# Optimization experiments

Hardware: AMD Instinct MI355X
Metric: run time of the kernel (lower is better)

The kernel has to match this reference:

```python
import jax, jax.numpy as jnp
import numpy as np
from jax.scipy.special import digamma, gammaln

B, NQ, NK, DM = 8, 2048, 2048, 64
NEG = -1e9


def setup_inputs() -> dict:
    key = jax.random.key(0)
    ks = jax.random.split(key, 9)
    y = jax.random.normal(ks[0], (B, NQ, DM), dtype=jnp.float32)
    x = jax.random.normal(ks[1], (B, NK, DM), dtype=jnp.float32)
    mask = jnp.ones((B, NQ, NK), dtype=jnp.float32)
    eps = jax.random.normal(ks[2], (B, NQ, NK), dtype=jnp.float32)
    # stacked 3-layer MLP params (all layers are DM x DM since d_q=d_k=d_v=d_m)
    Wq = jax.random.normal(ks[3], (3, DM, DM), dtype=jnp.float32) * 0.1
    bq = jnp.zeros((3, DM), dtype=jnp.float32)
    Wk = jax.random.normal(ks[4], (3, DM, DM), dtype=jnp.float32) * 0.1
    bk = jnp.zeros((3, DM), dtype=jnp.float32)
    Wv = jax.random.normal(ks[5], (3, DM, DM), dtype=jnp.float32) * 0.1
    bv = jnp.zeros((3, DM), dtype=jnp.float32)
    return {"y": y, "x": x, "mask": mask, "eps": eps,
            "Wq": Wq, "bq": bq, "Wk": Wk, "bk": bk, "Wv": Wv, "bv": bv}


def _mlp(h, W, b, last_softplus):
    # 3-layer MLP; softplus after first two layers, optionally after last
    for i in range(3):
        h = h @ W[i] + b[i]
        if i < 2 or last_softplus:
            h = jax.nn.softplus(h)
    return h


def _dirichlet_kld(alpha, mask):
    a0 = (alpha * mask).sum(-1, keepdims=True)
    dg_a = digamma(alpha)
    dg_a0 = digamma(a0)
    kl = (gammaln(a0)
          - (gammaln(alpha) * mask).sum(-1, keepdims=True)
          + (alpha * dg_a * mask).sum(-1, keepdims=True)
          - (alpha * dg_a0 * mask).sum(-1, keepdims=True)
          - ((dg_a - dg_a0) * mask).mean(-1, keepdims=True))
    return jnp.abs(kl)


def reference(y, x, mask, eps, Wq, bq, Wk, bk, Wv, bv):
    q = _mlp(y, Wq, bq, True)          # [B,NQ,DM]
    k = _mlp(x, Wk, bk, True)          # [B,NK,DM]
    va = _mlp(x, Wv, bv, False)        # [B,NK,DM]
    qk = jnp.einsum('bqd,bkd->bqk', q, k)
    alpha = qk + 1.0                   # > 1, safe for log/digamma
    log_alpha = jnp.log(alpha)
    mu = (log_alpha - (log_alpha * mask).mean(-1, keepdims=True)) * mask
    latent = mask.sum(-1, keepdims=True)
    inv_a = 1.0 / alpha
    sigma = ((1.0 - 2.0 / latent) * inv_a
             + (1.0 / latent ** 2) * (inv_a * mask).sum(-1, keepdims=True)) * mask
    kld = _dirichlet_kld(alpha, mask).mean()
    neg = (1.0 - mask) * NEG
    attn = jax.nn.softmax(mu + sigma * eps + neg, axis=-1)
    out = attn @ va                    # [B,NQ,DM]
    return out, attn, va, kld
```

## Files before the change

### kernel.cpp

```cpp
#include <hip/hip_runtime.h>
#include <cstdint>
#include <cstddef>

#define BB 8
#define NQ 2048
#define NK 2048
#define DM 64
#define QT 16
#define TPB 512
#define PST 2056

typedef float    f4    __attribute__((ext_vector_type(4)));
typedef short    s16x8 __attribute__((ext_vector_type(8)));
typedef unsigned u32x2 __attribute__((ext_vector_type(2)));
typedef unsigned u32x4 __attribute__((ext_vector_type(4)));

__device__ __forceinline__ float frcp(float x){
  float r = __builtin_amdgcn_rcpf(x);
  return r * (2.0f - x*r);
}
__device__ __forceinline__ float softplus(float v){
  return fmaxf(v, 0.0f) + log1pf(__expf(-fabsf(v)));
}
__device__ __forceinline__ float bflo(unsigned u){ return __uint_as_float(u << 16); }
__device__ __forceinline__ float bfhi(unsigned u){ return __uint_as_float(u & 0xffff0000u); }
__device__ __forceinline__ unsigned short f2bf(float f){
  unsigned u = __float_as_uint(f);
  return (unsigned short)((u + 0x7fffu + ((u >> 16) & 1u)) >> 16);
}
__device__ __forceinline__ unsigned pack_rne(float lo, float hi){
  return (unsigned)f2bf(lo) | ((unsigned)f2bf(hi) << 16);
}
__device__ __forceinline__ float red32(float v){
  #pragma unroll
  for (int s = 1; s < 32; s <<= 1) v += __shfl_xor(v, s);
  return v;
}

__global__ __launch_bounds__(256) void mlp3_kernel(
    const float* __restrict__ y, const float* __restrict__ x,
    const float* __restrict__ Wq, const float* __restrict__ bq,
    const float* __restrict__ Wk, const float* __restrict__ bk,
    const float* __restrict__ Wv, const float* __restrict__ bv,
    unsigned short* __restrict__ qo, unsigned short* __restrict__ ko,
    float* __restrict__ vo, unsigned short* __restrict__ vaT){
  const int which = blockIdx.y;
  const float* src = (which == 0) ? y : x;
  const float* W   = (which == 0) ? Wq : (which == 1 ? Wk : Wv);
  const float* bb  = (which == 0) ? bq : (which == 1 ? bk : bv);
  const int row0 = blockIdx.x * 64;
  const int t = threadIdx.x;
  const int lane = t & 63, w = t >> 6, lm = lane & 15, lg = lane >> 4;

  __shared__ unsigned short Xl[64][72];
  __shared__ unsigned short Wt[64][72];
  __shared__ float bl[64];

  #pragma unroll
  for (int p = 0; p < 4; ++p){
    int idx = t + p*256;
    int r = idx >> 4, c4 = idx & 15;
    f4 v = ((const f4*)(src + (size_t)row0*DM))[idx];
    u32x2 o = { pack_rne(v.x, v.y), pack_rne(v.z, v.w) };
    *(u32x2*)&Xl[r][c4*4] = o;
  }

  const int wr = w * 16;
  for (int l = 0; l < 3; ++l){
    __syncthreads();
    #pragma unroll
    for (int p = 0; p < 4; ++p){
      int idx = t + p*256;
      int k = idx >> 4, c4 = idx & 15;
      f4 v = ((const f4*)(W + l*DM*DM))[idx];
      Wt[c4*4+0][k] = f2bf(v.x);
      Wt[c4*4+1][k] = f2bf(v.y);
      Wt[c4*4+2][k] = f2bf(v.z);
      Wt[c4*4+3][k] = f2bf(v.w);
    }
    if (t < 64) bl[t] = bb[l*DM + t];
    __syncthreads();
    const bool sp = (l < 2) || (which != 2);
    s16x8 a0 = *(const s16x8*)&Xl[wr + lm][lg*8];
    s16x8 a1 = *(const s16x8*)&Xl[wr + lm][32 + lg*8];
    f4 outv[4];
    #pragma unroll
    for (int nt = 0; nt < 4; ++nt){
      s16x8 b0 = *(const s16x8*)&Wt[nt*16 + lm][lg*8];
      s16x8 b1 = *(const s16x8*)&Wt[nt*16 + lm][32 + lg*8];
      f4 acc = {0.f, 0.f, 0.f, 0.f};
      acc = __builtin_amdgcn_mfma_f32_16x16x32_bf16(a0, b0, acc, 0, 0, 0);
      acc = __builtin_amdgcn_mfma_f32_16x16x32_bf16(a1, b1, acc, 0, 0, 0);
      const float bc = bl[nt*16 + lm];
      #pragma unroll
      for (int r = 0; r < 4; ++r){
        float vv = acc[r] + bc;
        if (sp) vv = softplus(vv);
        acc[r] = vv;
      }
      outv[nt] = acc;
    }
    #pragma unroll
    for (int nt = 0; nt < 4; ++nt)
      #pragma unroll
      for (int r = 0; r < 4; ++r)
        Xl[wr + lg*4 + r][nt*16 + lm] = f2bf(outv[nt][r]);
  }
  __syncthreads();

  if (which != 2){
    unsigned short* dst = ((which == 0) ? qo : ko) + (size_t)row0*DM;
    #pragma unroll
    for (int p = 0; p < 4; ++p){
      int idx = t + p*256;
      int r = idx >> 4, c4 = idx & 15;
      u32x2 u = *(const u32x2*)&Xl[r][c4*4];
      *(u32x2*)(dst + (size_t)idx*4) = u;
    }
  } else {
    #pragma unroll
    for (int p = 0; p < 4; ++p){
      int idx = t + p*256;
      int r = idx >> 4, c4 = idx & 15;
      u32x2 u = *(const u32x2*)&Xl[r][c4*4];
      f4 v = { bflo(u[0]), bfhi(u[0]), bflo(u[1]), bfhi(u[1]) };
      ((f4*)(vo + (size_t)row0*DM))[idx] = v;
    }
    const int bidx = row0 >> 11, jb = row0 & 2047;
    const int d = t >> 2, rs = t & 3;
    u32x4 o0, o1;
    #pragma unroll
    for (int i = 0; i < 4; ++i)
      o0[i] = (unsigned)Xl[rs*16 + 2*i][d] | ((unsigned)Xl[rs*16 + 2*i + 1][d] << 16);
    #pragma unroll
    for (int i = 0; i < 4; ++i)
      o1[i] = (unsigned)Xl[rs*16 + 8 + 2*i][d] | ((unsigned)Xl[rs*16 + 9 + 2*i][d] << 16);
    unsigned short* dst = vaT + ((size_t)bidx*DM + d)*NK + jb + rs*16;
    *(u32x4*)dst       = o0;
    *(u32x4*)(dst + 8) = o1;
  }
}

__global__ __launch_bounds__(TPB, 4) void bayes_main_kernel(
    const unsigned short* __restrict__ qbf, const unsigned short* __restrict__ kbf,
    const unsigned short* __restrict__ vaT,
    const float* __restrict__ maskg, const float* __restrict__ epsg,
    float* __restrict__ outg, float* __restrict__ attng, float* __restrict__ klws){
  const int b  = blockIdx.x & 7;
  const int qt = blockIdx.x >> 3;
  const int q0 = qt * QT;
  const int t  = threadIdx.x;
  const int lane = t & 63, w = t >> 6;
  const int lm = lane & 15, lg = lane >> 4;

  __shared__ unsigned short Plds[QT][PST];
  __shared__ float pvred[4][QT][16];
  __shared__ float rowinvL[QT], klrow[QT];

  {
    const unsigned short* qrow = qbf + ((size_t)(b*NQ + q0 + lm))*DM + lg*8;
    s16x8 qa0 = *(const s16x8*)qrow;
    s16x8 qa1 = *(const s16x8*)(qrow + 32);
    #pragma unroll 2
    for (int tt = 0; tt < 16; ++tt){
      const int jt = w*16 + tt;
      const unsigned short* krow = kbf + ((size_t)(b*NK + jt*16 + lm))*DM + lg*8;
      s16x8 kb0 = *(const s16x8*)krow;
      s16x8 kb1 = *(const s16x8*)(krow + 32);
      f4 acc = {0.f, 0.f, 0.f, 0.f};
      acc = __builtin_amdgcn_mfma_f32_16x16x32_bf16(qa0, kb0, acc, 0, 0, 0);
      acc = __builtin_amdgcn_mfma_f32_16x16x32_bf16(qa1, kb1, acc, 0, 0, 0);
      #pragma unroll
      for (int r = 0; r < 4; ++r)
        Plds[lg*4 + r][jt*16 + lm] = f2bf(acc[r]);
    }
  }
  __syncthreads();

  const int row = t >> 5, c = t & 31;
  const size_t rowoff = ((size_t)(b*NQ) + q0 + row)*NK;

  float a0 = 0, Sg = 0, Sadg = 0, Sdg = 0, Sinv = 0, lat = 0;
  unsigned long long mbits = 0;
  #pragma unroll
  for (int h = 0; h < 2; ++h){
    f4 pm[8];
    #pragma unroll
    for (int k = 0; k < 8; ++k)
      pm[k] = *(const f4*)(maskg + rowoff + (h*8 + k)*128 + c*4);
    #pragma unroll
    for (int k = 0; k < 8; ++k){
      const int kk = h*8 + k;
      u32x2 sw = *(const u32x2*)&Plds[row][kk*128 + c*4];
      const float av[4] = { bflo(sw[0]) + 1.0f, bfhi(sw[0]) + 1.0f,
                            bflo(sw[1]) + 1.0f, bfhi(sw[1]) + 1.0f };
      #pragma unroll
      for (int c4 = 0; c4 < 4; ++c4){
        float a = av[c4], m = pm[k][c4];
        if (m != 0.0f) mbits |= 1ull << (kk*4 + c4);
        float inv = __builtin_amdgcn_rcpf(a);
        float la  = __logf(a);
        float xs  = a + 1.0f;
        float lxs = __logf(xs);
        float rxs = __builtin_amdgcn_rcpf(xs);
        float rx2 = rxs*rxs;
        float t1  = fmaf(-rx2, 1.0f/252.0f, 1.0f/120.0f);
        float t2  = fmaf(-rx2, t1, 1.0f/12.0f);
        float psi = fmaf(-rx2, t2, fmaf(-0.5f, rxs, lxs)) - inv;
        float u1  = fmaf(-rx2, 1.0f/1260.0f, 1.0f/360.0f);
        float u2  = fmaf(-rx2, u1, 1.0f/12.0f);
        float lg2 = fmaf(xs - 0.5f, lxs, fmaf(rxs, u2, 0.91893853320467274f))
                  - xs - la;
        a0   = fmaf(a,     m, a0);
        Sg   = fmaf(lg2,   m, Sg);
        Sadg = fmaf(a*psi, m, Sadg);
        Sdg  = fmaf(psi,   m, Sdg);
        Sinv = fmaf(inv,   m, Sinv);
        lat += m;
      }
    }
  }
  a0 = red32(a0); Sg = red32(Sg); Sadg = red32(Sadg);
  Sdg = red32(Sdg); Sinv = red32(Sinv); lat = red32(lat);

  const float invLT = frcp(lat);
  const float c1 = 1.0f - 2.0f*invLT;
  const float S2 = Sinv*invLT*invLT;
  if (c == 0){
    double A0d = (double)a0, csum = 0.0, prod = 1.0;
    #pragma unroll
    for (int s = 0; s < 7; ++s){
      if (A0d < 8.0){ csum += 1.0/A0d; prod *= A0d; A0d += 1.0; }
    }
    double lx = log(A0d), r1 = 1.0/A0d, r2 = r1*r1;
    double psiA = lx - 0.5*r1
                - r2*((1.0/12.0) - r2*((1.0/120.0) - r2*(1.0/252.0))) - csum;
    double lgA  = (A0d - 0.5)*lx - A0d + 0.918938533204672741
                + r1*((1.0/12.0) - r2*((1.0/360.0) - r2*(1.0/1260.0))) - log(prod);
    double kl = lgA - (double)Sg + (double)Sadg - psiA*(double)a0
              - ((double)Sdg - psiA*(double)lat)*(1.0/(double)NK);
    klrow[row] = (float)fabs(kl);
  }

  float esum = 0.0f;
  #pragma unroll
  for (int h = 0; h < 2; ++h){
    f4 pe[8];
    #pragma unroll
    for (int k = 0; k < 8; ++k)
      pe[k] = __builtin_nontemporal_load(
          (const f4*)(epsg + rowoff + (h*8 + k)*128 + c*4));
    #pragma unroll
    for (int k = 0; k < 8; ++k){
      const int kk = h*8 + k;
      u32x2 sw = *(const u32x2*)&Plds[row][kk*128 + c*4];
      const float av[4] = { bflo(sw[0]) + 1.0f, bfhi(sw[0]) + 1.0f,
                            bflo(sw[1]) + 1.0f, bfhi(sw[1]) + 1.0f };
      float e2v[4];
      #pragma unroll
      for (int c4 = 0; c4 < 4; ++c4){
        float e2 = 0.0f;
        if ((mbits >> (kk*4 + c4)) & 1ull){
          float a = av[c4];
          float sig = fmaf(c1, __builtin_amdgcn_rcpf(a), S2);
          e2 = a * __expf(sig * pe[k][c4]);
        }
        e2v[c4] = e2;
        esum += e2;
      }
      u32x2 ow = { pack_rne(e2v[0], e2v[1]), pack_rne(e2v[2], e2v[3]) };
      *(u32x2*)&Plds[row][kk*128 + c*4] = ow;
    }
  }
  esum = red32(esum);
  const float rinv = frcp(esum);
  if (c == 0) rowinvL[row] = rinv;

  #pragma unroll 4
  for (int k = 0; k < 16; ++k){
    u32x2 ew = *(const u32x2*)&Plds[row][k*128 + c*4];
    f4 o = { bflo(ew[0])*rinv, bfhi(ew[0])*rinv, bflo(ew[1])*rinv, bfhi(ew[1])*rinv };
    __builtin_nontemporal_store(o, (f4*)(attng + rowoff + k*128 + c*4));
  }
  __syncthreads();

  if (t == 0){
    float s = 0;
    #pragma unroll
    for (int r = 0; r < QT; ++r) s += klrow[r];
    klws[b*(NQ/QT) + qt] = s;
  }

  const int dt = w & 3, jh = w >> 2;
  f4 oacc = {0.f, 0.f, 0.f, 0.f};
  const unsigned short* vrow = vaT + ((size_t)(b*DM) + dt*16 + lm)*NK + jh*1024 + lg*8;
  const unsigned short* prow = &Plds[lm][jh*1024 + lg*8];
  #pragma unroll 4
  for (int ks = 0; ks < 32; ++ks){
    s16x8 pa = *(const s16x8*)(prow + ks*32);
    s16x8 vb = *(const s16x8*)(vrow + ks*32);
    oacc = __builtin_amdgcn_mfma_f32_16x16x32_bf16(pa, vb, oacc, 0, 0, 0);
  }
  if (w >= 4){
    #pragma unroll
    for (int r = 0; r < 4; ++r) pvred[dt][lg*4 + r][lm] = oacc[r];
  }
  __syncthreads();
  if (w < 4){
    #pragma unroll
    for (int r = 0; r < 4; ++r){
      const int q = lg*4 + r;
      float v = (oacc[r] + pvred[dt][q][lm]) * rowinvL[q];
      outg[((size_t)(b*NQ) + q0 + q)*DM + dt*16 + lm] = v;
    }
  }
}

__global__ __launch_bounds__(256) void kld_reduce_kernel(
    const float* __restrict__ klws, float* __restrict__ dst){
  float s = 0.0f;
  for (int i = threadIdx.x; i < BB*(NQ/QT); i += 256) s += klws[i];
  #pragma unroll
  for (int o = 32; o; o >>= 1) s += __shfl_down(s, o);
  __shared__ float w4[4];
  if ((threadIdx.x & 63) == 0) w4[threadIdx.x >> 6] = s;
  __syncthreads();
  if (threadIdx.x == 0)
    dst[0] = (w4[0] + w4[1] + w4[2] + w4[3]) * (1.0f/((float)BB*(float)NQ));
}

extern "C" void kernel_launch(void* const* d_in, const int* in_sizes, int n_in,
                              void* d_out, int out_size, void* d_ws, size_t ws_size,
                              hipStream_t stream){
  const float* y    = (const float*)d_in[0];
  const float* x    = (const float*)d_in[1];
  const float* mask = (const float*)d_in[2];
  const float* eps  = (const float*)d_in[3];
  const float* Wq   = (const float*)d_in[4];
  const float* bq   = (const float*)d_in[5];
  const float* Wk   = (const float*)d_in[6];
  const float* bk   = (const float*)d_in[7];
  const float* Wv   = (const float*)d_in[8];
  const float* bv   = (const float*)d_in[9];

  float* out  = (float*)d_out;
  float* attn = out  + (size_t)BB*NQ*DM;
  float* va   = attn + (size_t)BB*NQ*NK;
  float* kld  = va   + (size_t)BB*NK*DM;

  char* wsb = (char*)d_ws;
  unsigned short* qbf  = (unsigned short*)wsb;
  unsigned short* kbf  = (unsigned short*)(wsb + (size_t)BB*NQ*DM*2);
  unsigned short* vaT  = (unsigned short*)(wsb + (size_t)BB*NQ*DM*4);
  float*          klws = (float*)(wsb + (size_t)BB*NQ*DM*6);

  dim3 gA((BB*NQ)/64, 3);
  hipLaunchKernelGGL(mlp3_kernel, gA, dim3(256), 0, stream,
                     y, x, Wq, bq, Wk, bk, Wv, bv, qbf, kbf, va, vaT);
  hipLaunchKernelGGL(bayes_main_kernel, dim3(BB*(NQ/QT)), dim3(TPB), 0, stream,
                     qbf, kbf, vaT, mask, eps, out, attn, klws);
  hipLaunchKernelGGL(kld_reduce_kernel, dim3(1), dim3(256), 0, stream, klws, kld);
}
```

Measured before the change: 156.7 us.

## Replace per-element digamma/gammaln with aggregated Stirling sums and fold alpha+1 into bf16 store

```diff
diff --git a/kernel.cpp b/kernel.cpp
--- a/kernel.cpp
+++ b/kernel.cpp
@@ -10,6 +10,10 @@
 #define TPB 512
 #define PST 2056
 
+#define LN2f   0.6931471805599453f
+#define LOG2Ef 1.4426950408889634f
+#define HL2PIf 0.9189385332046727f
+
 typedef float    f4    __attribute__((ext_vector_type(4)));
 typedef short    s16x8 __attribute__((ext_vector_type(8)));
 typedef unsigned u32x2 __attribute__((ext_vector_type(2)));
@@ -30,6 +34,11 @@
 }
 __device__ __forceinline__ unsigned pack_rne(float lo, float hi){
   return (unsigned)f2bf(lo) | ((unsigned)f2bf(hi) << 16);
+}
+__device__ __forceinline__ unsigned cvtpk(float lo, float hi){
+  unsigned r;
+  asm("v_cvt_pk_bf16_f32 %0, %1, %2" : "=v"(r) : "v"(lo), "v"(hi));
+  return r;
 }
 __device__ __forceinline__ float red32(float v){
   #pragma unroll
@@ -170,9 +179,13 @@
       f4 acc = {0.f, 0.f, 0.f, 0.f};
       acc = __builtin_amdgcn_mfma_f32_16x16x32_bf16(qa0, kb0, acc, 0, 0, 0);
       acc = __builtin_amdgcn_mfma_f32_16x16x32_bf16(qa1, kb1, acc, 0, 0, 0);
-      #pragma unroll
-      for (int r = 0; r < 4; ++r)
-        Plds[lg*4 + r][jt*16 + lm] = f2bf(acc[r]);
+      unsigned p01 = cvtpk(acc[0] + 1.0f, acc[1] + 1.0f);
+      unsigned p23 = cvtpk(acc[2] + 1.0f, acc[3] + 1.0f);
+      const int col = jt*16 + lm;
+      Plds[lg*4 + 0][col] = (unsigned short)(p01 & 0xffffu);
+      Plds[lg*4 + 1][col] = (unsigned short)(p01 >> 16);
+      Plds[lg*4 + 2][col] = (unsigned short)(p23 & 0xffffu);
+      Plds[lg*4 + 3][col] = (unsigned short)(p23 >> 16);
     }
   }
   __syncthreads();
@@ -180,8 +193,7 @@
   const int row = t >> 5, c = t & 31;
   const size_t rowoff = ((size_t)(b*NQ) + q0 + row)*NK;
 
-  float a0 = 0, Sg = 0, Sadg = 0, Sdg = 0, Sinv = 0, lat = 0;
-  unsigned long long mbits = 0;
+  float a0 = 0, Sl2 = 0, Sinv = 0, Si2 = 0, lat = 0;
   #pragma unroll
   for (int h = 0; h < 2; ++h){
     f4 pm[8];
@@ -192,83 +204,71 @@
     for (int k = 0; k < 8; ++k){
       const int kk = h*8 + k;
       u32x2 sw = *(const u32x2*)&Plds[row][kk*128 + c*4];
-      const float av[4] = { bflo(sw[0]) + 1.0f, bfhi(sw[0]) + 1.0f,
-                            bflo(sw[1]) + 1.0f, bfhi(sw[1]) + 1.0f };
+      const float av[4] = { bflo(sw[0]), bfhi(sw[0]), bflo(sw[1]), bfhi(sw[1]) };
       #pragma unroll
       for (int c4 = 0; c4 < 4; ++c4){
         float a = av[c4], m = pm[k][c4];
-        if (m != 0.0f) mbits |= 1ull << (kk*4 + c4);
         float inv = __builtin_amdgcn_rcpf(a);
-        float la  = __logf(a);
-        float xs  = a + 1.0f;
-        float lxs = __logf(xs);
-        float rxs = __builtin_amdgcn_rcpf(xs);
-        float rx2 = rxs*rxs;
-        float t1  = fmaf(-rx2, 1.0f/252.0f, 1.0f/120.0f);
-        float t2  = fmaf(-rx2, t1, 1.0f/12.0f);
-        float psi = fmaf(-rx2, t2, fmaf(-0.5f, rxs, lxs)) - inv;
-        float u1  = fmaf(-rx2, 1.0f/1260.0f, 1.0f/360.0f);
-        float u2  = fmaf(-rx2, u1, 1.0f/12.0f);
-        float lg2 = fmaf(xs - 0.5f, lxs, fmaf(rxs, u2, 0.91893853320467274f))
-                  - xs - la;
-        a0   = fmaf(a,     m, a0);
-        Sg   = fmaf(lg2,   m, Sg);
-        Sadg = fmaf(a*psi, m, Sadg);
-        Sdg  = fmaf(psi,   m, Sdg);
-        Sinv = fmaf(inv,   m, Sinv);
+        float l2  = __builtin_amdgcn_logf(a);
+        a0   = fmaf(a,       m, a0);
+        Sl2  = fmaf(l2,      m, Sl2);
+        Sinv = fmaf(inv,     m, Sinv);
+        Si2  = fmaf(inv*inv, m, Si2);
         lat += m;
       }
     }
   }
-  a0 = red32(a0); Sg = red32(Sg); Sadg = red32(Sadg);
-  Sdg = red32(Sdg); Sinv = red32(Sinv); lat = red32(lat);
-
+  a0 = red32(a0); Sl2 = red32(Sl2); Sinv = red32(Sinv);
+  Si2 = red32(Si2); lat = red32(lat);
+
+  const float Sl = Sl2 * LN2f;
   const float invLT = frcp(lat);
   const float c1 = 1.0f - 2.0f*invLT;
   const float S2 = Sinv*invLT*invLT;
-  if (c == 0){
-    double A0d = (double)a0, csum = 0.0, prod = 1.0;
-    #pragma unroll
-    for (int s = 0; s < 7; ++s){
-      if (A0d < 8.0){ csum += 1.0/A0d; prod *= A0d; A0d += 1.0; }
-    }
-    double lx = log(A0d), r1 = 1.0/A0d, r2 = r1*r1;
-    double psiA = lx - 0.5*r1
-                - r2*((1.0/12.0) - r2*((1.0/120.0) - r2*(1.0/252.0))) - csum;
-    double lgA  = (A0d - 0.5)*lx - A0d + 0.918938533204672741
-                + r1*((1.0/12.0) - r2*((1.0/360.0) - r2*(1.0/1260.0))) - log(prod);
-    double kl = lgA - (double)Sg + (double)Sadg - psiA*(double)a0
-              - ((double)Sdg - psiA*(double)lat)*(1.0/(double)NK);
-    klrow[row] = (float)fabs(kl);
-  }
-
+  {
+    const float la0 = __builtin_amdgcn_logf(a0) * LN2f;
+    const float ra0 = frcp(a0);
+    const float ra2 = ra0*ra0;
+    const float psiA = la0 - 0.5f*ra0 - ra2*(1.0f/12.0f - ra2*(1.0f/120.0f));
+    const float lgA  = fmaf(a0 - 0.5f, la0, -a0) + HL2PIf
+                     + ra0*(1.0f/12.0f - ra2*(1.0f/360.0f));
+    const float gsum = fmaf(0.5f, Sl, a0) - lat*(0.5f + HL2PIf) - Sinv*(1.0f/6.0f);
+    const float Sdg  = Sl - 0.5f*Sinv - Si2*(1.0f/12.0f);
+    const float kl   = lgA - psiA*a0 + gsum
+                     - (Sdg - psiA*lat)*(1.0f/(float)NK);
+    if (c == 0) klrow[row] = fabsf(kl);
+  }
+
+  const float c1e = c1 * LOG2Ef, S2e = S2 * LOG2Ef;
   float esum = 0.0f;
-  #pragma unroll
-  for (int h = 0; h < 2; ++h){
-    f4 pe[8];
-    #pragma unroll
-    for (int k = 0; k < 8; ++k)
-      pe[k] = __builtin_nontemporal_load(
-          (const f4*)(epsg + rowoff + (h*8 + k)*128 + c*4));
-    #pragma unroll
-    for (int k = 0; k < 8; ++k){
-      const int kk = h*8 + k;
+  u32x2 e2pk[16];
+  #pragma unroll
+  for (int hb = 0; hb < 4; ++hb){
+    f4 pm[4], pe[4];
+    #pragma unroll
+    for (int j = 0; j < 4; ++j){
+      pm[j] = *(const f4*)(maskg + rowoff + (hb*4 + j)*128 + c*4);
+      pe[j] = __builtin_nontemporal_load(
+          (const f4*)(epsg + rowoff + (hb*4 + j)*128 + c*4));
+    }
+    #pragma unroll
+    for (int j = 0; j < 4; ++j){
+      const int kk = hb*4 + j;
       u32x2 sw = *(const u32x2*)&Plds[row][kk*128 + c*4];
-      const float av[4] = { bflo(sw[0]) + 1.0f, bfhi(sw[0]) + 1.0f,
-                            bflo(sw[1]) + 1.0f, bfhi(sw[1]) + 1.0f };
+      const float av[4] = { bflo(sw[0]), bfhi(sw[0]), bflo(sw[1]), bfhi(sw[1]) };
       float e2v[4];
       #pragma unroll
       for (int c4 = 0; c4 < 4; ++c4){
-        float e2 = 0.0f;
-        if ((mbits >> (kk*4 + c4)) & 1ull){
-          float a = av[c4];
-          float sig = fmaf(c1, __builtin_amdgcn_rcpf(a), S2);
-          e2 = a * __expf(sig * pe[k][c4]);
-        }
+        float a = av[c4];
+        float inv = __builtin_amdgcn_rcpf(a);
+        float zz = fmaf(c1e, inv, S2e) * pe[j][c4];
+        float p  = __builtin_amdgcn_exp2f(zz);
+        float e2 = a * p * pm[j][c4];
         e2v[c4] = e2;
         esum += e2;
       }
-      u32x2 ow = { pack_rne(e2v[0], e2v[1]), pack_rne(e2v[2], e2v[3]) };
+      u32x2 ow = { cvtpk(e2v[0], e2v[1]), cvtpk(e2v[2], e2v[3]) };
+      e2pk[kk] = ow;
       *(u32x2*)&Plds[row][kk*128 + c*4] = ow;
     }
   }
@@ -277,10 +277,10 @@
   if (c == 0) rowinvL[row] = rinv;
 
   #pragma unroll 4
-  for (int k = 0; k < 16; ++k){
-    u32x2 ew = *(const u32x2*)&Plds[row][k*128 + c*4];
+  for (int kk = 0; kk < 16; ++kk){
+    u32x2 ew = e2pk[kk];
     f4 o = { bflo(ew[0])*rinv, bfhi(ew[0])*rinv, bflo(ew[1])*rinv, bfhi(ew[1])*rinv };
-    __builtin_nontemporal_store(o, (f4*)(attng + rowoff + k*128 + c*4));
+    __builtin_nontemporal_store(o, (f4*)(attng + rowoff + kk*128 + c*4));
   }
   __syncthreads();
 
```

Result: no change. 157.2 us (+0.3%).
